# Performance work log

Measured on AMD Instinct MI355X. Metric: run time of the kernel, lower is better.

## Reference

```python
import jax, jax.numpy as jnp
import numpy as np

B, N, C, D, S, H = 64, 4096, 256, 256, 8, 512
ITERS = 3
EPS = 1e-8
LN_EPS = 1e-3
SCALE = D ** -0.5


def _ln(x, g, b):
    mu = jnp.mean(x, axis=-1, keepdims=True)
    var = jnp.mean((x - mu) ** 2, axis=-1, keepdims=True)
    return (x - mu) * jax.lax.rsqrt(var + LN_EPS) * g + b


def setup_inputs() -> dict:
    key = jax.random.key(0)
    ks = jax.random.split(key, 16)
    limit = np.sqrt(6.0 / (1 + D))
    d = {
        "inputs": jax.random.normal(ks[0], (B, N, C), jnp.float32),
        "noise": jax.random.normal(ks[1], (B, S, D), jnp.float32),
        "slots_mu": jax.random.uniform(ks[2], (1, 1, D), jnp.float32, -limit, limit),
        "slots_log_sigma": jax.random.uniform(ks[3], (1, 1, D), jnp.float32, -limit, limit),
        "Wq": jax.random.normal(ks[4], (D, D), jnp.float32) * (D ** -0.5),
        "Wk": jax.random.normal(ks[5], (D, C), jnp.float32) * (C ** -0.5),
        "Wv": jax.random.normal(ks[6], (D, C), jnp.float32) * (C ** -0.5),
        "W_ih": jax.random.normal(ks[7], (3 * D, D), jnp.float32) * (D ** -0.5),
        "W_hh": jax.random.normal(ks[8], (3 * D, D), jnp.float32) * (D ** -0.5),
        "b_ih": jnp.zeros((3 * D,), jnp.float32),
        "b_hh": jnp.zeros((3 * D,), jnp.float32),
        "mlp_W1": jax.random.normal(ks[9], (H, D), jnp.float32) * (D ** -0.5),
        "mlp_b1": jnp.zeros((H,), jnp.float32),
        "mlp_W2": jax.random.normal(ks[10], (D, H), jnp.float32) * (H ** -0.5),
        "mlp_b2": jnp.zeros((D,), jnp.float32),
        "ln_in_g": jnp.ones((C,), jnp.float32), "ln_in_b": jnp.zeros((C,), jnp.float32),
        "ln_s_g": jnp.ones((D,), jnp.float32), "ln_s_b": jnp.zeros((D,), jnp.float32),
        "ln_ff_g": jnp.ones((D,), jnp.float32), "ln_ff_b": jnp.zeros((D,), jnp.float32),
    }
    return d


def reference(inputs, noise, slots_mu, slots_log_sigma, Wq, Wk, Wv,
              W_ih, W_hh, b_ih, b_hh, mlp_W1, mlp_b1, mlp_W2, mlp_b2,
              ln_in_g, ln_in_b, ln_s_g, ln_s_b, ln_ff_g, ln_ff_b):
    # slot init: mu + exp(log_sigma) * noise  (torch.normal reparameterized)
    slots = slots_mu + jnp.exp(slots_log_sigma) * noise  # [B,S,D]
    x = _ln(inputs, ln_in_g, ln_in_b)
    k = jnp.einsum('bnc,dc->bnd', x, Wk)  # [B,N,D]
    v = jnp.einsum('bnc,dc->bnd', x, Wv)  # [B,N,D]

    for _ in range(ITERS):
        slots_prev = slots
        s = _ln(slots, ln_s_g, ln_s_b)
        q = jnp.einsum('bsd,ed->bse', s, Wq)
        dots = jnp.einsum('bsd,bnd->bsn', q, k) * SCALE  # [B,S,N]
        attn = jax.nn.softmax(dots, axis=1) + EPS  # softmax over SLOT dim
        attn = attn / jnp.sum(attn, axis=-1, keepdims=True)
        updates = jnp.einsum('bnd,bsn->bsd', v, attn)  # [B,S,D]
        # GRUCell(updates, slots_prev)
        gx = updates @ W_ih.T + b_ih  # [B,S,3D]
        gh = slots_prev @ W_hh.T + b_hh
        xr, xz, xn = jnp.split(gx, 3, axis=-1)
        hr, hz, hn = jnp.split(gh, 3, axis=-1)
        r = jax.nn.sigmoid(xr + hr)
        z = jax.nn.sigmoid(xz + hz)
        n = jnp.tanh(xn + r * hn)
        slots = (1.0 - z) * n + z * slots_prev
        # MLP residual
        p = _ln(slots, ln_ff_g, ln_ff_b)
        h1 = jax.nn.relu(p @ mlp_W1.T + mlp_b1)
        slots = slots + h1 @ mlp_W2.T + mlp_b2
    return slots
```

## Files before the change

kernel.cpp:

```cpp
#include <hip/hip_runtime.h>

typedef unsigned short u16;
typedef unsigned int u32;
typedef __attribute__((ext_vector_type(4))) float f32x4;
typedef __attribute__((ext_vector_type(8))) short s16x8;

#define GM 262144
#define GB 64
#define GN 4096
#define GS 8
#define NPART 16

#define GLDS16(G, L) __builtin_amdgcn_global_load_lds( \
    (const __attribute__((address_space(1))) void*)(G), \
    (__attribute__((address_space(3))) void*)(L), 16, 0, 0)

__device__ __forceinline__ float bf2f(u16 u) {
  union { unsigned int i; float f; } c; c.i = ((unsigned int)u) << 16; return c.f;
}
__device__ __forceinline__ u16 f2bf(float f) {
  union { float f; unsigned int i; } c; c.f = f;
  unsigned int x = c.i;
  unsigned int r = x + 0x7FFFu + ((x >> 16) & 1u);
  return (u16)(r >> 16);
}
__device__ __forceinline__ float dot4(f32x4 a, f32x4 b) {
  return a.x*b.x + a.y*b.y + a.z*b.z + a.w*b.w;
}

__global__ void init_slots_kernel(const float* __restrict__ noise, const float* __restrict__ smu,
                                  const float* __restrict__ sls, float* __restrict__ slots)
{
  int i = blockIdx.x * 256 + threadIdx.x;
  int d = i & 255;
  slots[i] = smu[d] + expf(sls[d]) * noise[i];
}

__global__ void wprep_kernel(const float* __restrict__ Wk, const float* __restrict__ Wv,
                             const float* __restrict__ Wih, const float* __restrict__ Whh,
                             const float* __restrict__ W1, const float* __restrict__ W2,
                             u16* __restrict__ wkv, u16* __restrict__ Wcat,
                             u16* __restrict__ W1b, u16* __restrict__ W2b)
{
  int i = blockIdx.x * 256 + threadIdx.x;
  if (i < 131072) {
    wkv[i] = f2bf(i < 65536 ? Wk[i] : Wv[i - 65536]);
  } else if (i < 655360) {
    int j2 = i - 131072;
    int r = j2 >> 9, k = j2 & 511;
    float v;
    if (r < 512)      v = (k < 256) ? Wih[r * 256 + k] : Whh[r * 256 + (k - 256)];
    else if (r < 768) v = (k < 256) ? Wih[r * 256 + k] : 0.f;
    else              v = (k < 256) ? 0.f : Whh[(r - 256) * 256 + (k - 256)];
    Wcat[j2] = f2bf(v);
  } else if (i < 786432) {
    W1b[i - 655360] = f2bf(W1[i - 655360]);
  } else {
    W2b[i - 786432] = f2bf(W2[i - 786432]);
  }
}

__global__ __launch_bounds__(256) void wqk_kernel(
    const float* __restrict__ Wk, const float* __restrict__ Wq,
    float* __restrict__ WqkT, u16* __restrict__ WqkTb)
{
  __shared__ float wkc[256];
  int c = blockIdx.x, t = threadIdx.x;
  wkc[t] = Wk[t * 256 + c];
  __syncthreads();
  float a0 = 0.f, a1 = 0.f, a2 = 0.f, a3 = 0.f;
  #pragma unroll 4
  for (int d = 0; d < 256; d += 4) {
    a0 += wkc[d]     * Wq[(d)     * 256 + t];
    a1 += wkc[d + 1] * Wq[(d + 1) * 256 + t];
    a2 += wkc[d + 2] * Wq[(d + 2) * 256 + t];
    a3 += wkc[d + 3] * Wq[(d + 3) * 256 + t];
  }
  float acc = (a0 + a1 + a2 + a3) * 0.0625f;
  WqkT[c * 256 + t] = acc;
  WqkTb[c * 256 + t] = f2bf(acc);
}

__global__ __launch_bounds__(256) void ln_bf16_kernel(
    const float* __restrict__ x, const float* __restrict__ g, const float* __restrict__ be,
    u16* __restrict__ xbuf)
{
  int row = blockIdx.x * 4 + (threadIdx.x >> 6);
  int lane = threadIdx.x & 63;
  f32x4 v = *(const f32x4*)&x[(size_t)row * 256 + lane * 4];
  float s = v.x + v.y + v.z + v.w;
  float sq = v.x*v.x + v.y*v.y + v.z*v.z + v.w*v.w;
  #pragma unroll
  for (int m = 1; m < 64; m <<= 1) { s += __shfl_xor(s, m, 64); sq += __shfl_xor(sq, m, 64); }
  float mu = s * (1.f / 256.f);
  float var = sq * (1.f / 256.f) - mu * mu;
  float rstd = rsqrtf(var + 1e-3f);
  f32x4 gv = *(const f32x4*)&g[lane * 4];
  f32x4 bv = *(const f32x4*)&be[lane * 4];
  uint2 pk;
  pk.x = (u32)f2bf((v.x - mu) * rstd * gv.x + bv.x)
       | ((u32)f2bf((v.y - mu) * rstd * gv.y + bv.y) << 16);
  pk.y = (u32)f2bf((v.z - mu) * rstd * gv.z + bv.z)
       | ((u32)f2bf((v.w - mu) * rstd * gv.w + bv.w) << 16);
  *(uint2*)&xbuf[(size_t)row * 256 + lane * 4] = pk;
}

__global__ __launch_bounds__(256) void qproj_kernel(const float* __restrict__ slots,
    const float* __restrict__ WqkT,
    const float* __restrict__ g, const float* __restrict__ be, float* __restrict__ gqk)
{
  __shared__ __align__(16) float sl[8][256];
  int b = blockIdx.x, t = threadIdx.x;
  int lane = t & 63, w = t >> 6;
  #pragma unroll
  for (int s2 = 0; s2 < 2; ++s2) {
    int s = w * 2 + s2;
    f32x4 v = *(const f32x4*)&slots[(size_t)(b * 8 + s) * 256 + lane * 4];
    float s1 = v.x + v.y + v.z + v.w;
    float q1 = v.x*v.x + v.y*v.y + v.z*v.z + v.w*v.w;
    #pragma unroll
    for (int m = 1; m < 64; m <<= 1) { s1 += __shfl_xor(s1, m, 64); q1 += __shfl_xor(q1, m, 64); }
    float mu = s1 * (1.f / 256.f);
    float var = q1 * (1.f / 256.f) - mu * mu;
    float rstd = rsqrtf(var + 1e-3f);
    f32x4 gv = *(const f32x4*)&g[lane * 4];
    f32x4 bv = *(const f32x4*)&be[lane * 4];
    f32x4 o;
    o.x = (v.x - mu) * rstd * gv.x + bv.x;
    o.y = (v.y - mu) * rstd * gv.y + bv.y;
    o.z = (v.z - mu) * rstd * gv.z + bv.z;
    o.w = (v.w - mu) * rstd * gv.w + bv.w;
    *(f32x4*)&sl[s][lane * 4] = o;
  }
  __syncthreads();
  float a[8];
  #pragma unroll
  for (int s = 0; s < 8; ++s) a[s] = 0.f;
  const f32x4* wr = (const f32x4*)&WqkT[(size_t)t * 256];
  for (int k = 0; k < 64; ++k) {
    f32x4 w4 = wr[k];
    #pragma unroll
    for (int s = 0; s < 8; ++s) a[s] += dot4(w4, *(const f32x4*)&sl[s][k * 4]);
  }
  #pragma unroll
  for (int s = 0; s < 8; ++s) gqk[(size_t)(b * 8 + s) * 256 + t] = a[s];
}

__global__ __launch_bounds__(256) void attn_kernel(
    const u16* __restrict__ xb, const float* __restrict__ gqk,
    float* __restrict__ gUp, float* __restrict__ gdp)
{
  __shared__ __align__(16) u16 X[64 * 256];
  __shared__ __align__(16) u16 P[16 * 72];
  __shared__ float denL[4][8];
  const int b = blockIdx.y, chunk = blockIdx.x;
  const int t = threadIdx.x;
  const int lane = t & 63, w = t >> 6;
  const int fr = lane & 15, fq = lane >> 4;
  const bool valid = fr < 8;

  for (int i = t; i < 288; i += 256) ((u32*)P)[288 + i] = 0;

  s16x8 qf[8];
  if (valid) {
    const float* qr = gqk + (size_t)b * 2048 + fr * 256;
    #pragma unroll
    for (int ks = 0; ks < 8; ++ks) {
      f32x4 a = *(const f32x4*)&qr[ks * 32 + fq * 8];
      f32x4 c = *(const f32x4*)&qr[ks * 32 + fq * 8 + 4];
      s16x8 q8;
      q8[0] = (short)f2bf(a.x); q8[1] = (short)f2bf(a.y);
      q8[2] = (short)f2bf(a.z); q8[3] = (short)f2bf(a.w);
      q8[4] = (short)f2bf(c.x); q8[5] = (short)f2bf(c.y);
      q8[6] = (short)f2bf(c.z); q8[7] = (short)f2bf(c.w);
      qf[ks] = q8;
    }
  } else {
    #pragma unroll
    for (int ks = 0; ks < 8; ++ks) { s16x8 z = {0,0,0,0,0,0,0,0}; qf[ks] = z; }
  }

  const int fnA = ((fr >> 1) & 4) | ((w & 1) << 1);
  const int fnB = ((fq & 1) << 2) | ((fq >> 1) << 1);

  float denom_loc = 0.f;
  f32x4 uacc[4];
  #pragma unroll
  for (int ct = 0; ct < 4; ++ct) { f32x4 z = {0.f,0.f,0.f,0.f}; uacc[ct] = z; }

  for (int ti = 0; ti < 4; ++ti) {
    const u16* src = xb + ((size_t)b * 4096 + (size_t)(chunk * 4 + ti) * 64) * 256;
    __syncthreads();
    #pragma unroll
    for (int p = 0; p < 8; ++p) {
      int q = p * 256 + t;
      int n = q >> 5, cl = q & 31;
      int fn = ((n >> 1) & 4) | ((n >> 3) & 2);
      GLDS16(src + (size_t)n * 256 + ((cl ^ fn) * 8), &X[q * 8]);
    }
    asm volatile("s_waitcnt vmcnt(0)");
    __syncthreads();

    f32x4 dacc = {0.f, 0.f, 0.f, 0.f};
    {
      const u16* xrow = &X[(w * 16 + fr) * 256];
      #pragma unroll
      for (int ks = 0; ks < 8; ++ks) {
        s16x8 a = *(const s16x8*)&xrow[(((ks * 4 + fq) ^ fnA) * 8)];
        dacc = __builtin_amdgcn_mfma_f32_16x16x32_bf16(a, qf[ks], dacc, 0, 0, 0);
      }
    }
    float pw[4];
    #pragma unroll
    for (int r = 0; r < 4; ++r) {
      float d = dacc[r];
      float m = d;
      #pragma unroll
      for (int msk = 1; msk < 8; msk <<= 1) m = fmaxf(m, __shfl_xor(m, msk, 64));
      float e = expf(d - m);
      float sm = e;
      #pragma unroll
      for (int msk = 1; msk < 8; msk <<= 1) sm += __shfl_xor(sm, msk, 64);
      pw[r] = valid ? (e / sm + 1e-8f) : 0.f;
    }
    denom_loc += pw[0] + pw[1] + pw[2] + pw[3];
    if (valid) {
      u32* p32 = (u32*)P;
      int pi = fr * 36 + w * 8 + fq * 2;
      p32[pi]     = (u32)f2bf(pw[0]) | ((u32)f2bf(pw[1]) << 16);
      p32[pi + 1] = (u32)f2bf(pw[2]) | ((u32)f2bf(pw[3]) << 16);
    }
    __syncthreads();

    #pragma unroll
    for (int ch = 0; ch < 2; ++ch) {
      s16x8 pa = *(const s16x8*)&P[fr * 72 + ch * 32 + fq * 8];
      #pragma unroll
      for (int ct = 0; ct < 4; ++ct) {
        int c = w * 64 + ct * 16 + fr;
        const u16* xcol = &X[(ch * 32 + fq * 8) * 256 + (((c >> 3) ^ fnB) * 8) + (c & 7)];
        union { s16x8 v; u32 u[4]; } vb;
        #pragma unroll
        for (int jj = 0; jj < 4; ++jj) {
          u16 e0 = xcol[(jj * 2) * 256];
          u16 e1 = xcol[(jj * 2 + 1) * 256];
          vb.u[jj] = (u32)e0 | ((u32)e1 << 16);
        }
        uacc[ct] = __builtin_amdgcn_mfma_f32_16x16x32_bf16(pa, vb.v, uacc[ct], 0, 0, 0);
      }
    }
  }

  float dl = denom_loc;
  dl += __shfl_xor(dl, 16, 64);
  dl += __shfl_xor(dl, 32, 64);
  if (lane < 8) denL[w][lane] = dl;
  if (fq < 2) {
    size_t obase = (size_t)(b * NPART + chunk) * 2048;
    #pragma unroll
    for (int ct = 0; ct < 4; ++ct)
      #pragma unroll
      for (int r = 0; r < 4; ++r)
        gUp[obase + (size_t)(fq * 4 + r) * 256 + w * 64 + ct * 16 + fr] = uacc[ct][r];
  }
  __syncthreads();
  if (t < 8) gdp[(b * NPART + chunk) * 8 + t] = denL[0][t] + denL[1][t] + denL[2][t] + denL[3][t];
}

__global__ __launch_bounds__(256) void update_kernel(
    const float* __restrict__ gUp, const float* __restrict__ gdp,
    float* __restrict__ slots,
    const u16* __restrict__ WvB,
    const u16* __restrict__ Wcat, const float* __restrict__ b_ih, const float* __restrict__ b_hh,
    const u16* __restrict__ W1b, const float* __restrict__ b1,
    const u16* __restrict__ W2b, const float* __restrict__ b2,
    const float* __restrict__ lng, const float* __restrict__ lnb,
    const u16* __restrict__ WqkTb, const float* __restrict__ lnsg, const float* __restrict__ lnsb,
    float* __restrict__ gqk, float* __restrict__ out, int last)
{
  __shared__ __align__(16) u16 bufA[16 * 520];
  __shared__ __align__(16) u16 bufP[16 * 264];
  __shared__ __align__(16) u16 bufU[16 * 264];
  __shared__ float g[1024 * 10];
  __shared__ float nl[8 * 256];
  __shared__ float sp[8 * 256];
  __shared__ float scr[16];
  const int b = blockIdx.x;
  const int t = threadIdx.x;
  const int lane = t & 63, w = t >> 6;
  const int fr = lane & 15, fq = lane >> 4;

  #pragma unroll
  for (int s = 0; s < 8; ++s) {
    float den = 0.f, ua = 0.f;
    #pragma unroll 4
    for (int c = 0; c < NPART; ++c) {
      den += gdp[(b * NPART + c) * 8 + s];
      ua  += gUp[(size_t)(b * NPART + c) * 2048 + s * 256 + t];
    }
    bufU[s * 264 + t] = f2bf(ua / den);
    float spv = slots[(b * 8 + s) * 256 + t];
    bufA[s * 520 + 256 + t] = f2bf(spv);
    sp[s * 256 + t] = spv;
  }
  for (int i = t; i < 8 * 520; i += 256) bufA[8 * 520 + i] = 0;
  for (int i = t; i < 8 * 264; i += 256) { bufP[8 * 264 + i] = 0; bufU[8 * 264 + i] = 0; }
  __syncthreads();

  {
    s16x8 pa[8];
    #pragma unroll
    for (int ks = 0; ks < 8; ++ks)
      pa[ks] = *(const s16x8*)&bufU[fr * 264 + ks * 32 + fq * 8];
    for (int nf = 0; nf < 4; ++nf) {
      int n0 = w * 64 + nf * 16;
      f32x4 acc = {0.f, 0.f, 0.f, 0.f};
      #pragma unroll
      for (int ks = 0; ks < 8; ++ks) {
        s16x8 bb = *(const s16x8*)&WvB[(size_t)(n0 + fr) * 256 + ks * 32 + fq * 8];
        acc = __builtin_amdgcn_mfma_f32_16x16x32_bf16(pa[ks], bb, acc, 0, 0, 0);
      }
      if (fq < 2) {
        int d = n0 + fr;
        #pragma unroll
        for (int r = 0; r < 4; ++r)
          bufA[(fq * 4 + r) * 520 + d] = f2bf(acc[r]);
      }
    }
  }
  __syncthreads();

  {
    s16x8 afr[16];
    #pragma unroll
    for (int ks = 0; ks < 16; ++ks)
      afr[ks] = *(const s16x8*)&bufA[fr * 520 + ks * 32 + fq * 8];
    for (int nf = 0; nf < 16; ++nf) {
      int n0 = w * 256 + nf * 16;
      f32x4 acc = {0.f, 0.f, 0.f, 0.f};
      #pragma unroll
      for (int ks = 0; ks < 16; ++ks) {
        s16x8 bb = *(const s16x8*)&Wcat[(size_t)(n0 + fr) * 512 + ks * 32 + fq * 8];
        acc = __builtin_amdgcn_mfma_f32_16x16x32_bf16(afr[ks], bb, acc, 0, 0, 0);
      }
      if (fq < 2) {
        int j = n0 + fr;
        #pragma unroll
        for (int r = 0; r < 4; ++r) g[j * 10 + fq * 4 + r] = acc[r];
      }
    }
  }
  __syncthreads();

  {
    float bi0 = b_ih[t],       bh0 = b_hh[t];
    float bi1 = b_ih[256 + t], bh1 = b_hh[256 + t];
    float bi2 = b_ih[512 + t], bh2 = b_hh[512 + t];
    #pragma unroll
    for (int s = 0; s < 8; ++s) {
      float rr = 1.f / (1.f + expf(-(g[t * 10 + s] + bi0 + bh0)));
      float z  = 1.f / (1.f + expf(-(g[(256 + t) * 10 + s] + bi1 + bh1)));
      float xn = g[(512 + t) * 10 + s] + bi2;
      float hn = g[(768 + t) * 10 + s] + bh2;
      float nn = tanhf(xn + rr * hn);
      nl[s * 256 + t] = (1.f - z) * nn + z * sp[s * 256 + t];
    }
  }
  __syncthreads();

  {
    int ln_ = t & 63;
    #pragma unroll
    for (int j = 0; j < 2; ++j) {
      int sl = w * 2 + j;
      f32x4 v = *(const f32x4*)&nl[sl * 256 + ln_ * 4];
      float s1 = v.x + v.y + v.z + v.w;
      float s2 = v.x*v.x + v.y*v.y + v.z*v.z + v.w*v.w;
      #pragma unroll
      for (int m = 1; m < 64; m <<= 1) { s1 += __shfl_xor(s1, m, 64); s2 += __shfl_xor(s2, m, 64); }
      if (ln_ == 0) {
        float mu = s1 * (1.f / 256.f);
        float var = s2 * (1.f / 256.f) - mu * mu;
        scr[sl * 2] = mu;
        scr[sl * 2 + 1] = rsqrtf(var + 1e-3f);
      }
    }
  }
  __syncthreads();
  {
    float lg = lng[t], lb = lnb[t];
    #pragma unroll
    for (int s = 0; s < 8; ++s)
      bufP[s * 264 + t] = f2bf((nl[s * 256 + t] - scr[s * 2]) * scr[s * 2 + 1] * lg + lb);
  }
  __syncthreads();

  {
    s16x8 pa[8];
    #pragma unroll
    for (int ks = 0; ks < 8; ++ks)
      pa[ks] = *(const s16x8*)&bufP[fr * 264 + ks * 32 + fq * 8];
    for (int nf = 0; nf < 8; ++nf) {
      int n0 = w * 128 + nf * 16;
      f32x4 acc = {0.f, 0.f, 0.f, 0.f};
      #pragma unroll
      for (int ks = 0; ks < 8; ++ks) {
        s16x8 bb = *(const s16x8*)&W1b[(size_t)(n0 + fr) * 256 + ks * 32 + fq * 8];
        acc = __builtin_amdgcn_mfma_f32_16x16x32_bf16(pa[ks], bb, acc, 0, 0, 0);
      }
      if (fq < 2) {
        float bb1 = b1[n0 + fr];
        #pragma unroll
        for (int r = 0; r < 4; ++r)
          bufA[(fq * 4 + r) * 520 + n0 + fr] = f2bf(fmaxf(acc[r] + bb1, 0.f));
      }
    }
  }
  __syncthreads();

  {
    s16x8 ha[16];
    #pragma unroll
    for (int ks = 0; ks < 16; ++ks)
      ha[ks] = *(const s16x8*)&bufA[fr * 520 + ks * 32 + fq * 8];
    for (int nf = 0; nf < 4; ++nf) {
      int n0 = w * 64 + nf * 16;
      f32x4 acc = {0.f, 0.f, 0.f, 0.f};
      #pragma unroll
      for (int ks = 0; ks < 16; ++ks) {
        s16x8 bb = *(const s16x8*)&W2b[(size_t)(n0 + fr) * 512 + ks * 32 + fq * 8];
        acc = __builtin_amdgcn_mfma_f32_16x16x32_bf16(ha[ks], bb, acc, 0, 0, 0);
      }
      if (fq < 2) {
        int d = n0 + fr;
        float bb2 = b2[d];
        #pragma unroll
        for (int r = 0; r < 4; ++r) {
          int sl = fq * 4 + r;
          float val = acc[r] + nl[sl * 256 + d] + bb2;
          slots[(b * 8 + sl) * 256 + d] = val;
          sp[sl * 256 + d] = val;
          if (last) out[(b * 8 + sl) * 256 + d] = val;
        }
      }
    }
  }
  if (last) return;
  __syncthreads();

  {
    int ln_ = t & 63;
    #pragma unroll
    for (int j = 0; j < 2; ++j) {
      int sl = w * 2 + j;
      f32x4 v = *(const f32x4*)&sp[sl * 256 + ln_ * 4];
      float s1 = v.x + v.y + v.z + v.w;
      float s2 = v.x*v.x + v.y*v.y + v.z*v.z + v.w*v.w;
      #pragma unroll
      for (int m = 1; m < 64; m <<= 1) { s1 += __shfl_xor(s1, m, 64); s2 += __shfl_xor(s2, m, 64); }
      if (ln_ == 0) {
        float mu = s1 * (1.f / 256.f);
        float var = s2 * (1.f / 256.f) - mu * mu;
        scr[sl * 2] = mu;
        scr[sl * 2 + 1] = rsqrtf(var + 1e-3f);
      }
    }
  }
  __syncthreads();
  {
    float lg = lnsg[t], lb = lnsb[t];
    #pragma unroll
    for (int s = 0; s < 8; ++s)
      bufP[s * 264 + t] = f2bf((sp[s * 256 + t] - scr[s * 2]) * scr[s * 2 + 1] * lg + lb);
  }
  __syncthreads();
  {
    s16x8 pa[8];
    #pragma unroll
    for (int ks = 0; ks < 8; ++ks)
      pa[ks] = *(const s16x8*)&bufP[fr * 264 + ks * 32 + fq * 8];
    for (int nf = 0; nf < 4; ++nf) {
      int n0 = w * 64 + nf * 16;
      f32x4 acc = {0.f, 0.f, 0.f, 0.f};
      #pragma unroll
      for (int ks = 0; ks < 8; ++ks) {
        s16x8 bb = *(const s16x8*)&WqkTb[(size_t)(n0 + fr) * 256 + ks * 32 + fq * 8];
        acc = __builtin_amdgcn_mfma_f32_16x16x32_bf16(pa[ks], bb, acc, 0, 0, 0);
      }
      if (fq < 2) {
        int e = n0 + fr;
        #pragma unroll
        for (int r = 0; r < 4; ++r)
          gqk[(size_t)(b * 8 + fq * 4 + r) * 256 + e] = acc[r];
      }
    }
  }
}

extern "C" void kernel_launch(void* const* d_in, const int* in_sizes, int n_in,
                              void* d_out, int out_size, void* d_ws, size_t ws_size,
                              hipStream_t stream) {
  const float* inputs   = (const float*)d_in[0];
  const float* noise    = (const float*)d_in[1];
  const float* slots_mu = (const float*)d_in[2];
  const float* slots_ls = (const float*)d_in[3];
  const float* Wq   = (const float*)d_in[4];
  const float* Wk   = (const float*)d_in[5];
  const float* Wv   = (const float*)d_in[6];
  const float* W_ih = (const float*)d_in[7];
  const float* W_hh = (const float*)d_in[8];
  const float* b_ih = (const float*)d_in[9];
  const float* b_hh = (const float*)d_in[10];
  const float* W1   = (const float*)d_in[11];
  const float* b1   = (const float*)d_in[12];
  const float* W2   = (const float*)d_in[13];
  const float* b2   = (const float*)d_in[14];
  const float* ln_in_g = (const float*)d_in[15];
  const float* ln_in_b = (const float*)d_in[16];
  const float* ln_s_g  = (const float*)d_in[17];
  const float* ln_s_b  = (const float*)d_in[18];
  const float* ln_ff_g = (const float*)d_in[19];
  const float* ln_ff_b = (const float*)d_in[20];
  float* out = (float*)d_out;

  char* w = (char*)d_ws;
  u16* xbuf = (u16*)w;      w += (size_t)GM * 256 * 2;
  float* gUp = (float*)w;
  float* gdp = (float*)(w + (size_t)GB * NPART * 2048 * 4);
  w += (size_t)GB * NPART * 2048 * 4 + (size_t)GB * NPART * 8 * 4 + 4096;
  u16* wkv = (u16*)w;       w += (size_t)512 * 256 * 2;
  u16* Wcat = (u16*)w;      w += (size_t)1024 * 512 * 2;
  u16* W1b = (u16*)w;       w += (size_t)512 * 256 * 2;
  u16* W2b = (u16*)w;       w += (size_t)256 * 512 * 2;
  float* WqkT = (float*)w;  w += (size_t)256 * 256 * 4;
  u16* WqkTb = (u16*)w;     w += (size_t)256 * 256 * 2;
  float* slots = (float*)w; w += (size_t)131072 * 4;
  float* gqk = (float*)w;   w += (size_t)131072 * 4;

  u16* WvB = wkv + 65536;

  init_slots_kernel<<<512, 256, 0, stream>>>(noise, slots_mu, slots_ls, slots);
  wprep_kernel<<<3584, 256, 0, stream>>>(Wk, Wv, W_ih, W_hh, W1, W2, wkv, Wcat, W1b, W2b);
  wqk_kernel<<<256, 256, 0, stream>>>(Wk, Wq, WqkT, WqkTb);
  ln_bf16_kernel<<<GM / 4, 256, 0, stream>>>(inputs, ln_in_g, ln_in_b, xbuf);

  qproj_kernel<<<64, 256, 0, stream>>>(slots, WqkT, ln_s_g, ln_s_b, gqk);
  for (int it = 0; it < 3; ++it) {
    attn_kernel<<<dim3(NPART, GB), 256, 0, stream>>>(xbuf, gqk, gUp, gdp);
    update_kernel<<<64, 256, 0, stream>>>(gUp, gdp, slots, WvB, Wcat, b_ih, b_hh,
                                          W1b, b1, W2b, b2, ln_ff_g, ln_ff_b,
                                          WqkTb, ln_s_g, ln_s_b, gqk, out, it == 2);
  }
}
```

Measured before the change: 494.9 us.

## Double-buffer X tiles in attention kernel to overlap global loads with MFMA

```diff
diff --git a/kernel.cpp b/kernel.cpp
--- a/kernel.cpp
+++ b/kernel.cpp
@@ -150,7 +150,7 @@
     const u16* __restrict__ xb, const float* __restrict__ gqk,
     float* __restrict__ gUp, float* __restrict__ gdp)
 {
-  __shared__ __align__(16) u16 X[64 * 256];
+  __shared__ __align__(16) u16 X[2 * 64 * 256];
   __shared__ __align__(16) u16 P[16 * 72];
   __shared__ float denL[4][8];
   const int b = blockIdx.y, chunk = blockIdx.x;
@@ -160,6 +160,17 @@
   const bool valid = fr < 8;
 
   for (int i = t; i < 288; i += 256) ((u32*)P)[288 + i] = 0;
+
+  {
+    const u16* src = xb + ((size_t)b * 4096 + (size_t)(chunk * 4) * 64) * 256;
+    #pragma unroll
+    for (int p = 0; p < 8; ++p) {
+      int q = p * 256 + t;
+      int n = q >> 5, cl = q & 31;
+      int fn = ((n >> 1) & 4) | ((n >> 3) & 2);
+      GLDS16(src + (size_t)n * 256 + ((cl ^ fn) * 8), &X[q * 8]);
+    }
+  }
 
   s16x8 qf[8];
   if (valid) {
@@ -188,22 +199,33 @@
   #pragma unroll
   for (int ct = 0; ct < 4; ++ct) { f32x4 z = {0.f,0.f,0.f,0.f}; uacc[ct] = z; }
 
+  #pragma unroll
   for (int ti = 0; ti < 4; ++ti) {
-    const u16* src = xb + ((size_t)b * 4096 + (size_t)(chunk * 4 + ti) * 64) * 256;
-    __syncthreads();
-    #pragma unroll
-    for (int p = 0; p < 8; ++p) {
-      int q = p * 256 + t;
-      int n = q >> 5, cl = q & 31;
-      int fn = ((n >> 1) & 4) | ((n >> 3) & 2);
-      GLDS16(src + (size_t)n * 256 + ((cl ^ fn) * 8), &X[q * 8]);
-    }
-    asm volatile("s_waitcnt vmcnt(0)");
-    __syncthreads();
+    __builtin_amdgcn_s_barrier();
+    __builtin_amdgcn_sched_barrier(0);
+    if (ti < 3) {
+      const u16* src = xb + ((size_t)b * 4096 + (size_t)(chunk * 4 + ti + 1) * 64) * 256;
+      u16* dstb = &X[((ti + 1) & 1) * 16384];
+      #pragma unroll
+      for (int p = 0; p < 8; ++p) {
+        int q = p * 256 + t;
+        int n = q >> 5, cl = q & 31;
+        int fn = ((n >> 1) & 4) | ((n >> 3) & 2);
+        GLDS16(src + (size_t)n * 256 + ((cl ^ fn) * 8), dstb + q * 8);
+      }
+      asm volatile("s_waitcnt vmcnt(8)" ::: "memory");
+    } else {
+      asm volatile("s_waitcnt vmcnt(0)" ::: "memory");
+    }
+    __builtin_amdgcn_sched_barrier(0);
+    __builtin_amdgcn_s_barrier();
+    __builtin_amdgcn_sched_barrier(0);
+
+    const u16* Xc = &X[(ti & 1) * 16384];
 
     f32x4 dacc = {0.f, 0.f, 0.f, 0.f};
     {
-      const u16* xrow = &X[(w * 16 + fr) * 256];
+      const u16* xrow = &Xc[(w * 16 + fr) * 256];
       #pragma unroll
       for (int ks = 0; ks < 8; ++ks) {
         s16x8 a = *(const s16x8*)&xrow[(((ks * 4 + fq) ^ fnA) * 8)];
@@ -230,7 +252,10 @@
       p32[pi]     = (u32)f2bf(pw[0]) | ((u32)f2bf(pw[1]) << 16);
       p32[pi + 1] = (u32)f2bf(pw[2]) | ((u32)f2bf(pw[3]) << 16);
     }
-    __syncthreads();
+    asm volatile("s_waitcnt lgkmcnt(0)" ::: "memory");
+    __builtin_amdgcn_sched_barrier(0);
+    __builtin_amdgcn_s_barrier();
+    __builtin_amdgcn_sched_barrier(0);
 
     #pragma unroll
     for (int ch = 0; ch < 2; ++ch) {
@@ -238,7 +263,7 @@
       #pragma unroll
       for (int ct = 0; ct < 4; ++ct) {
         int c = w * 64 + ct * 16 + fr;
-        const u16* xcol = &X[(ch * 32 + fq * 8) * 256 + (((c >> 3) ^ fnB) * 8) + (c & 7)];
+        const u16* xcol = &Xc[(ch * 32 + fq * 8) * 256 + (((c >> 3) ^ fnB) * 8) + (c & 7)];
         union { s16x8 v; u32 u[4]; } vb;
         #pragma unroll
         for (int jj = 0; jj < 4; ++jj) {
```

Result: slower. 512.2 us (+3.5%).
